# Kernel tuning notes

Hardware: AMD Instinct MI355X
Metric: run time of the kernel (lower is better)

The kernel has to match this reference:

```python
import jax, jax.numpy as jnp
import numpy as np

D = 256
BN_EPS = 1e-5
EPS = 0.0  # GINEEConv eps buffer, train_eps=False


def setup_inputs() -> dict:
    key = jax.random.key(0)
    ks = jax.random.split(key, 16)
    N, E, G = 60000, 200000, 1500
    node_features = jax.random.normal(ks[0], (N, 92), dtype=jnp.float32)
    edge_index = jax.random.randint(ks[1], (2, E), 0, N)
    atom_weights = jax.random.normal(ks[2], (E, 1), dtype=jnp.float32)
    batch = jnp.sort(jax.random.randint(ks[3], (N,), 0, G))
    s = 0.05
    return {
        "node_features": node_features,
        "edge_index": edge_index,
        "atom_weights": atom_weights,
        "batch": batch,
        "aW": jax.random.normal(ks[4], (92, D), dtype=jnp.float32) * s,
        "ab": jnp.zeros((D,), jnp.float32),
        "eW": jax.random.normal(ks[5], (1, D), dtype=jnp.float32) * s,
        "eb": jnp.zeros((D,), jnp.float32),
        "mlpW": jax.random.normal(ks[6], (3 * D, D), dtype=jnp.float32) * s,
        "mlpb": jnp.zeros((D,), jnp.float32),
        "nnW": jax.random.normal(ks[7], (D, D), dtype=jnp.float32) * s,
        "nnb": jnp.zeros((D,), jnp.float32),
        "bn_g": jax.random.normal(ks[8], (D,), dtype=jnp.float32) * 0.1 + 1.0,
        "bn_b": jax.random.normal(ks[9], (D,), dtype=jnp.float32) * 0.1,
        "bn_m": jax.random.normal(ks[10], (D,), dtype=jnp.float32) * 0.1,
        "bn_v": jax.random.uniform(ks[11], (D,), dtype=jnp.float32) + 0.5,
        "outW": jax.random.normal(ks[12], (D, 6), dtype=jnp.float32) * s,
        "outb": jnp.zeros((6,), jnp.float32),
    }


def _gine_layer(x, e_attr, row, col, mlpW, mlpb, nnW, nnb, bn_g, bn_b, bn_m, bn_v):
    # mlp(cat[x[row], x[col], e_attr]) without materializing the [E,3D] concat
    W1, W2, W3 = mlpW[:D], mlpW[D:2 * D], mlpW[2 * D:]
    new_e = x[row] @ W1 + x[col] @ W2 + e_attr @ W3 + mlpb  # [E, D]
    # message: relu(x_j + edge_attr), x_j = source nodes = edge_index[0]
    msg = jax.nn.relu(x[row] + new_e)  # [E, D]
    agg = jax.ops.segment_sum(msg, col, num_segments=x.shape[0])  # scatter-add to targets
    out = agg + (1.0 + EPS) * x  # residual
    h = out @ nnW + nnb
    h = (h - bn_m) * jax.lax.rsqrt(bn_v + BN_EPS) * bn_g + bn_b  # BN (eval stats)
    return jax.nn.relu(h), new_e


def reference(node_features, edge_index, atom_weights, batch,
              aW, ab, eW, eb, mlpW, mlpb, nnW, nnb,
              bn_g, bn_b, bn_m, bn_v, outW, outb):
    row, col = edge_index[0], edge_index[1]
    x = node_features @ aW + ab            # [N, 256]
    e_attr = atom_weights @ eW + eb        # [E, 256]
    for _ in range(4):  # 4 layers SHARING the same params (ModuleList of same module)
        x, e_attr = _gine_layer(x, e_attr, row, col, mlpW, mlpb, nnW, nnb,
                                bn_g, bn_b, bn_m, bn_v)
    pooled = jax.ops.segment_sum(x, batch, num_segments=1500)  # global_add_pool
    return pooled @ outW + outb  # [G, 6]
```

## Files before the change

### kernel.cpp

```cpp
#include <hip/hip_runtime.h>
#include <stdint.h>

#define DD 256
#define NNODE 60000
#define MPAD 60032
#define NEDGE 200000
#define NGRAPH 1500
#define NCHUNK 59

typedef __bf16 bf16x8 __attribute__((ext_vector_type(8)));
typedef float f32x4 __attribute__((ext_vector_type(4)));
typedef unsigned short us8 __attribute__((ext_vector_type(8)));

__device__ __forceinline__ unsigned short f2bf(float f) {
    union { float f; unsigned int u; } v; v.f = f;
    unsigned int r = v.u + 0x7FFFu + ((v.u >> 16) & 1u);
    return (unsigned short)(r >> 16);
}
__device__ __forceinline__ float bf2f(unsigned short h) {
    union { unsigned int u; float f; } v; v.u = ((unsigned int)h) << 16;
    return v.f;
}
__device__ __forceinline__ void gload_lds16(const void* g, void* l) {
    __builtin_amdgcn_global_load_lds((const __attribute__((address_space(1))) void*)g,
                                     (__attribute__((address_space(3))) void*)l, 16, 0, 0);
}

__global__ __launch_bounds__(256) void prep_weights(const float* __restrict__ mlpW,
                                                    const float* __restrict__ nnW,
                                                    const float* __restrict__ aW,
                                                    const float* __restrict__ ab,
                                                    unsigned short* __restrict__ wc1,
                                                    unsigned short* __restrict__ wc2,
                                                    unsigned short* __restrict__ nnt,
                                                    unsigned short* __restrict__ aWt) {
    int idx = blockIdx.x * 256 + threadIdx.x;
    if (idx < 256 * 512) {
        int n = idx >> 9, k = idx & 511;
        float v1 = (k < 256) ? mlpW[k * DD + n] : mlpW[(k + 256) * DD + n];
        wc1[idx] = f2bf(v1);
        wc2[idx] = f2bf(mlpW[(k + 256) * DD + n]);
    }
    if (idx < 256 * 256) {
        int n = idx >> 8, k = idx & 255;
        nnt[idx] = f2bf(nnW[k * DD + n]);
    }
    if (idx < 256 * 96) {
        int n = idx / 96, k = idx - n * 96;
        float v = (k < 92) ? aW[k * DD + n] : (k == 92 ? ab[n] : 0.0f);
        aWt[idx] = f2bf(v);
    }
}

__global__ __launch_bounds__(256) void prep_uv(const float* __restrict__ eW, const float* __restrict__ eb,
                                               const float* __restrict__ mlpW, const float* __restrict__ mlpb,
                                               const float* __restrict__ nnb,
                                               const float* __restrict__ bn_g, const float* __restrict__ bn_b,
                                               const float* __restrict__ bn_m, const float* __restrict__ bn_v,
                                               float* __restrict__ u_all, float* __restrict__ v_all,
                                               float* __restrict__ scale, float* __restrict__ shift) {
    __shared__ float uc[DD], vc[DD];
    int d = threadIdx.x;
    uc[d] = eW[d];
    vc[d] = eb[d];
    float sc = bn_g[d] * rsqrtf(bn_v[d] + 1e-5f);
    scale[d] = sc;
    shift[d] = (nnb[d] - bn_m[d]) * sc + bn_b[d];
    __syncthreads();
    const float* W3 = mlpW + 2 * DD * DD;
    for (int it = 0; it < 4; ++it) {
        float su = 0.f, sv = 0.f;
        for (int k = 0; k < DD; ++k) {
            float w = W3[k * DD + d];
            su += uc[k] * w;
            sv += vc[k] * w;
        }
        sv += mlpb[d];
        u_all[it * DD + d] = su;
        v_all[it * DD + d] = sv;
        __syncthreads();
        uc[d] = su; vc[d] = sv;
        __syncthreads();
    }
}

__global__ __launch_bounds__(256) void nfb_prep(const float* __restrict__ nf, unsigned short* __restrict__ nfb) {
    int idx = blockIdx.x * 256 + threadIdx.x;
    if (idx >= MPAD * 96) return;
    int r = idx / 96, c = idx - r * 96;
    float v;
    if (r < NNODE && c < 92) v = nf[(size_t)r * 92 + c];
    else v = (c == 92) ? 1.0f : 0.0f;
    nfb[idx] = f2bf(v);
}

__global__ __launch_bounds__(512) void xinit_gemm(const unsigned short* __restrict__ nfb,
                                                  const unsigned short* __restrict__ aWt,
                                                  unsigned short* __restrict__ x) {
    __shared__ unsigned short As[128][96];
    __shared__ unsigned short Bs[256][96];
    const int tid = threadIdx.x;
    const int lane = tid & 63, wid = tid >> 6;
    const int wr = wid >> 2, wc = wid & 3;
    const int m0 = blockIdx.x * 128;
    const int lr = lane & 15, lq = lane >> 4;

    for (int i = tid; i < 128 * 12; i += 512) {
        int row = i / 12, ch = (i - row * 12) * 8;
        gload_lds16(nfb + (size_t)(m0 + row) * 96 + ch, &As[row][ch]);
    }
    for (int i = tid; i < 256 * 12; i += 512) {
        int row = i / 12, ch = (i - row * 12) * 8;
        gload_lds16(aWt + (size_t)row * 96 + ch, &Bs[row][ch]);
    }
    __syncthreads();

    f32x4 acc[4][4];
    #pragma unroll
    for (int m = 0; m < 4; ++m)
        #pragma unroll
        for (int n = 0; n < 4; ++n) { f32x4 z = {0.f,0.f,0.f,0.f}; acc[m][n] = z; }

    #pragma unroll
    for (int h = 0; h < 3; ++h) {
        bf16x8 af[4], bf[4];
        #pragma unroll
        for (int m = 0; m < 4; ++m)
            af[m] = *reinterpret_cast<const bf16x8*>(&As[wr * 64 + m * 16 + lr][h * 32 + lq * 8]);
        #pragma unroll
        for (int n = 0; n < 4; ++n)
            bf[n] = *reinterpret_cast<const bf16x8*>(&Bs[wc * 64 + n * 16 + lr][h * 32 + lq * 8]);
        #pragma unroll
        for (int m = 0; m < 4; ++m)
            #pragma unroll
            for (int n = 0; n < 4; ++n)
                acc[m][n] = __builtin_amdgcn_mfma_f32_16x16x32_bf16(af[m], bf[n], acc[m][n], 0, 0, 0);
    }

    #pragma unroll
    for (int m = 0; m < 4; ++m) {
        const int rb = m0 + wr * 64 + m * 16 + lq * 4;
        #pragma unroll
        for (int n = 0; n < 4; ++n) {
            const int c = wc * 64 + n * 16 + lr;
            #pragma unroll
            for (int j = 0; j < 4; ++j)
                x[(size_t)(rb + j) * DD + c] = f2bf(acc[m][n][j]);
        }
    }
}

__global__ __launch_bounds__(256) void hist_kernel(const int* __restrict__ ei, int* __restrict__ counts) {
    int e = blockIdx.x * 256 + threadIdx.x;
    if (e < NEDGE) atomicAdd(&counts[ei[NEDGE + e]], 1);
}

__global__ __launch_bounds__(256) void scan1(const int* __restrict__ counts, int* __restrict__ blockSums) {
    int t = threadIdx.x;
    int base = blockIdx.x * 1024 + t * 4;
    int s = 0;
    #pragma unroll
    for (int i = 0; i < 4; ++i) { int idx = base + i; if (idx < NNODE) s += counts[idx]; }
    __shared__ int red[256];
    red[t] = s; __syncthreads();
    for (int d = 128; d; d >>= 1) { if (t < d) red[t] += red[t + d]; __syncthreads(); }
    if (t == 0) blockSums[blockIdx.x] = red[0];
}

__global__ __launch_bounds__(64) void scan2(int* __restrict__ blockSums) {
    int t = threadIdx.x;
    int v = (t < NCHUNK) ? blockSums[t] : 0;
    int orig = v;
    #pragma unroll
    for (int d = 1; d < 64; d <<= 1) {
        int o = __shfl_up(v, d);
        if (t >= d) v += o;
    }
    if (t < NCHUNK) blockSums[t] = v - orig;
}

__global__ __launch_bounds__(256) void scan3(const int* __restrict__ counts, const int* __restrict__ blockSums,
                                             int* __restrict__ offsets, int* __restrict__ cursor) {
    int t = threadIdx.x;
    int base = blockIdx.x * 1024 + t * 4;
    int c[4]; int s = 0;
    #pragma unroll
    for (int i = 0; i < 4; ++i) { int idx = base + i; c[i] = (idx < NNODE) ? counts[idx] : 0; s += c[i]; }
    __shared__ int lds[256];
    lds[t] = s; __syncthreads();
    for (int d = 1; d < 256; d <<= 1) {
        int v = (t >= d) ? lds[t - d] : 0;
        __syncthreads();
        lds[t] += v;
        __syncthreads();
    }
    int off = blockSums[blockIdx.x] + lds[t] - s;
    #pragma unroll
    for (int i = 0; i < 4; ++i) {
        int idx = base + i;
        if (idx < NNODE) { offsets[idx] = off; cursor[idx] = off; off += c[i]; }
    }
}

__global__ __launch_bounds__(256) void scatter_kernel(const int* __restrict__ ei, const float* __restrict__ aw,
                                                      int* __restrict__ cursor,
                                                      int* __restrict__ srow, float* __restrict__ sw) {
    int e = blockIdx.x * 256 + threadIdx.x;
    if (e < NEDGE) {
        int c = ei[NEDGE + e];
        int pos = atomicAdd(&cursor[c], 1);
        srow[pos] = ei[e];
        sw[pos] = aw[e];
    }
}

template <int EPI>
__global__ __launch_bounds__(512) void gemm_kernel(
    const unsigned short* __restrict__ A0,
    const unsigned short* __restrict__ A1,
    const unsigned short* __restrict__ Bt, int btStride, int Ktot,
    unsigned short* __restrict__ Cout,
    const float* __restrict__ scale, const float* __restrict__ shift) {
    __shared__ unsigned short As[128][64];
    __shared__ unsigned short Bs[256][64];
    const int tid = threadIdx.x;
    const int lane = tid & 63, wid = tid >> 6;
    const int wr = wid >> 2, wc = wid & 3;
    const int m0 = blockIdx.x * 128;
    const int lr = lane & 15, lq = lane >> 4;
    const int srow = tid >> 3;
    const int jphys = tid & 7;
    const int jlog = jphys ^ (srow & 7);
    const int scol_g = jlog * 8;
    const int scol_l = jphys * 8;
    const int xorj = (lr & 7);

    f32x4 acc[4][4];
    #pragma unroll
    for (int m = 0; m < 4; ++m)
        #pragma unroll
        for (int n = 0; n < 4; ++n) { f32x4 z = {0.f,0.f,0.f,0.f}; acc[m][n] = z; }

    const int nk = Ktot >> 6;
    for (int kt = 0; kt < nk; ++kt) {
        const int k0 = kt << 6;
        const unsigned short* Ap; int ka;
        if (k0 < 256) { Ap = A0; ka = k0; } else { Ap = A1; ka = k0 - 256; }
        #pragma unroll
        for (int p = 0; p < 2; ++p) {
            int row = p * 64 + srow;
            gload_lds16(Ap + (size_t)(m0 + row) * DD + ka + scol_g, &As[row][scol_l]);
        }
        #pragma unroll
        for (int p = 0; p < 4; ++p) {
            int row = p * 64 + srow;
            gload_lds16(Bt + (size_t)row * btStride + k0 + scol_g, &Bs[row][scol_l]);
        }
        __syncthreads();
        #pragma unroll
        for (int h = 0; h < 2; ++h) {
            const int jp = ((h * 4 + lq) ^ xorj) * 8;
            bf16x8 af[4], bfr[4];
            #pragma unroll
            for (int m = 0; m < 4; ++m)
                af[m] = *reinterpret_cast<const bf16x8*>(&As[wr * 64 + m * 16 + lr][jp]);
            #pragma unroll
            for (int n = 0; n < 4; ++n)
                bfr[n] = *reinterpret_cast<const bf16x8*>(&Bs[wc * 64 + n * 16 + lr][jp]);
            #pragma unroll
            for (int m = 0; m < 4; ++m)
                #pragma unroll
                for (int n = 0; n < 4; ++n)
                    acc[m][n] = __builtin_amdgcn_mfma_f32_16x16x32_bf16(af[m], bfr[n], acc[m][n], 0, 0, 0);
        }
        __syncthreads();
    }

    #pragma unroll
    for (int m = 0; m < 4; ++m) {
        const int rb = m0 + wr * 64 + m * 16 + lq * 4;
        #pragma unroll
        for (int n = 0; n < 4; ++n) {
            const int c = wc * 64 + n * 16 + lr;
            #pragma unroll
            for (int j = 0; j < 4; ++j) {
                const size_t idx = (size_t)(rb + j) * DD + c;
                if (EPI == 0) {
                    Cout[idx] = f2bf(acc[m][n][j]);
                } else {
                    float y = fmaxf(acc[m][n][j] * scale[c] + shift[c], 0.f);
                    Cout[idx] = f2bf(y);
                }
            }
        }
    }
}

__global__ __launch_bounds__(256) void edge_csr(const int* __restrict__ offsets, const int* __restrict__ counts,
                                                const int* __restrict__ srow, const float* __restrict__ sw,
                                                const unsigned short* __restrict__ X,
                                                const unsigned short* __restrict__ P,
                                                const unsigned short* __restrict__ Q,
                                                const float* __restrict__ u, const float* __restrict__ v,
                                                unsigned short* __restrict__ aggB) {
    const int lane = threadIdx.x & 63, wid = threadIdx.x >> 6;
    const int n = blockIdx.x * 4 + wid;
    if (n >= NNODE) return;
    const int start = offsets[n];
    const int deg = counts[n];
    const int sub = lane & 31, h = lane >> 5;

    const us8* X8 = (const us8*)X;
    const us8* P8 = (const us8*)P;

    float4 u0 = ((const float4*)u)[sub * 2], u1 = ((const float4*)u)[sub * 2 + 1];
    float4 v0 = ((const float4*)v)[sub * 2], v1 = ((const float4*)v)[sub * 2 + 1];
    float uu[8] = {u0.x, u0.y, u0.z, u0.w, u1.x, u1.y, u1.z, u1.w};
    float vv[8] = {v0.x, v0.y, v0.z, v0.w, v1.x, v1.y, v1.z, v1.w};

    us8 qv = ((const us8*)Q)[(size_t)n * 32 + sub];
    float base[8];
    #pragma unroll
    for (int c = 0; c < 8; ++c) base[c] = bf2f(qv[c]) + vv[c];

    float a[8];
    us8 xv = X8[(size_t)n * 32 + sub];
    #pragma unroll
    for (int c = 0; c < 8; ++c) a[c] = (h == 0) ? bf2f(xv[c]) : 0.f;

    for (int b0 = 0; b0 < deg; b0 += 64) {
        int m = deg - b0; if (m > 64) m = 64;
        int myr = 0; float myw = 0.f;
        if (lane < m) { myr = srow[start + b0 + lane]; myw = sw[start + b0 + lane]; }
        int iters = (m + 1) >> 1;
        for (int j = 0; j < iters; ++j) {
            int el = 2 * j + h;
            int r = __shfl(myr, el);
            float w = __shfl(myw, el);
            if (el < m) {
                us8 x2 = X8[(size_t)r * 32 + sub];
                us8 p2 = P8[(size_t)r * 32 + sub];
                #pragma unroll
                for (int c = 0; c < 8; ++c)
                    a[c] += fmaxf(bf2f(x2[c]) + bf2f(p2[c]) + base[c] + w * uu[c], 0.f);
            }
        }
    }
    #pragma unroll
    for (int c = 0; c < 8; ++c) a[c] += __shfl_xor(a[c], 32);
    if (h == 0) {
        us8 o;
        #pragma unroll
        for (int c = 0; c < 8; ++c) o[c] = f2bf(a[c]);
        ((us8*)aggB)[(size_t)n * 32 + sub] = o;
    }
}

__global__ __launch_bounds__(256) void pool_kernel(const unsigned short* __restrict__ x,
                                                   const int* __restrict__ batch,
                                                   float* __restrict__ pooled) {
    const int lane = threadIdx.x & 63, wid = threadIdx.x >> 6;
    const int base = (blockIdx.x * 4 + wid) * 8;
    float4 acc = make_float4(0.f, 0.f, 0.f, 0.f);
    int gcur = -1;
    for (int i = 0; i < 8; ++i) {
        int n = base + i;
        if (n >= NNODE) break;
        int g = batch[n];
        if (g != gcur) {
            if (gcur >= 0) {
                float* pp = pooled + (size_t)gcur * DD + lane * 4;
                unsafeAtomicAdd(pp + 0, acc.x);
                unsafeAtomicAdd(pp + 1, acc.y);
                unsafeAtomicAdd(pp + 2, acc.z);
                unsafeAtomicAdd(pp + 3, acc.w);
            }
            gcur = g;
            acc = make_float4(0.f, 0.f, 0.f, 0.f);
        }
        ushort4 xv = ((const ushort4*)x)[(size_t)n * 64 + lane];
        acc.x += bf2f(xv.x); acc.y += bf2f(xv.y);
        acc.z += bf2f(xv.z); acc.w += bf2f(xv.w);
    }
    if (gcur >= 0) {
        float* pp = pooled + (size_t)gcur * DD + lane * 4;
        unsafeAtomicAdd(pp + 0, acc.x);
        unsafeAtomicAdd(pp + 1, acc.y);
        unsafeAtomicAdd(pp + 2, acc.z);
        unsafeAtomicAdd(pp + 3, acc.w);
    }
}

__global__ __launch_bounds__(64) void out_kernel(const float* __restrict__ pooled,
                                                 const float* __restrict__ outW,
                                                 const float* __restrict__ outb,
                                                 float* __restrict__ out) {
    const int g = blockIdx.x, lane = threadIdx.x;
    float4 p = ((const float4*)pooled)[g * 64 + lane];
    float s[6];
    #pragma unroll
    for (int j = 0; j < 6; ++j) {
        float a = p.x * outW[(lane * 4 + 0) * 6 + j] + p.y * outW[(lane * 4 + 1) * 6 + j] +
                  p.z * outW[(lane * 4 + 2) * 6 + j] + p.w * outW[(lane * 4 + 3) * 6 + j];
        #pragma unroll
        for (int off = 32; off; off >>= 1) a += __shfl_down(a, off);
        s[j] = a;
    }
    if (lane == 0) {
        #pragma unroll
        for (int j = 0; j < 6; ++j) out[g * 6 + j] = s[j] + outb[j];
    }
}

extern "C" void kernel_launch(void* const* d_in, const int* in_sizes, int n_in,
                              void* d_out, int out_size, void* d_ws, size_t ws_size,
                              hipStream_t stream) {
    const float* nf    = (const float*)d_in[0];
    const int*   ei    = (const int*)d_in[1];
    const float* aw    = (const float*)d_in[2];
    const int*   batch = (const int*)d_in[3];
    const float* aW    = (const float*)d_in[4];
    const float* ab    = (const float*)d_in[5];
    const float* eW    = (const float*)d_in[6];
    const float* eb    = (const float*)d_in[7];
    const float* mlpW  = (const float*)d_in[8];
    const float* mlpb  = (const float*)d_in[9];
    const float* nnW   = (const float*)d_in[10];
    const float* nnb   = (const float*)d_in[11];
    const float* bn_g  = (const float*)d_in[12];
    const float* bn_b  = (const float*)d_in[13];
    const float* bn_m  = (const float*)d_in[14];
    const float* bn_v  = (const float*)d_in[15];
    const float* outW  = (const float*)d_in[16];
    const float* outb  = (const float*)d_in[17];
    float* out = (float*)d_out;

    char* ws = (char*)d_ws;
    size_t off = 0;
    auto alloc = [&](size_t bytes) -> void* {
        void* p = ws + off;
        off += (bytes + 255) & ~(size_t)255;
        return p;
    };
    unsigned short* x    = (unsigned short*)alloc((size_t)MPAD * DD * 2);
    unsigned short* P    = (unsigned short*)alloc((size_t)MPAD * DD * 2);
    unsigned short* Q    = (unsigned short*)alloc((size_t)MPAD * DD * 2);
    unsigned short* aggB = (unsigned short*)alloc((size_t)MPAD * DD * 2);
    unsigned short* nfb  = (unsigned short*)alloc((size_t)MPAD * 96 * 2);
    unsigned short* wc1  = (unsigned short*)alloc(256 * 512 * 2);
    unsigned short* wc2  = (unsigned short*)alloc(256 * 512 * 2);
    unsigned short* nnt  = (unsigned short*)alloc(256 * 256 * 2);
    unsigned short* aWt  = (unsigned short*)alloc(256 * 96 * 2);
    float* u_all = (float*)alloc(4 * DD * 4);
    float* v_all = (float*)alloc(4 * DD * 4);
    float* scale = (float*)alloc(DD * 4);
    float* shift = (float*)alloc(DD * 4);
    float* pooled = (float*)alloc((size_t)NGRAPH * DD * 4);
    int* counts  = (int*)alloc((size_t)NNODE * 4);
    int* offsets = (int*)alloc((size_t)NNODE * 4);
    int* cursor  = (int*)alloc((size_t)NNODE * 4);
    int* blockSums = (int*)alloc(NCHUNK * 4);
    int* srowB   = (int*)alloc((size_t)NEDGE * 4);
    float* swB   = (float*)alloc((size_t)NEDGE * 4);
    (void)ws_size; (void)in_sizes; (void)n_in; (void)out_size;

    prep_weights<<<512, 256, 0, stream>>>(mlpW, nnW, aW, ab, wc1, wc2, nnt, aWt);
    prep_uv<<<1, 256, 0, stream>>>(eW, eb, mlpW, mlpb, nnb, bn_g, bn_b, bn_m, bn_v,
                                   u_all, v_all, scale, shift);
    nfb_prep<<<(MPAD * 96 + 255) / 256, 256, 0, stream>>>(nf, nfb);
    xinit_gemm<<<MPAD / 128, 512, 0, stream>>>(nfb, aWt, x);

    hipMemsetAsync(counts, 0, (size_t)NNODE * 4, stream);
    hist_kernel<<<(NEDGE + 255) / 256, 256, 0, stream>>>(ei, counts);
    scan1<<<NCHUNK, 256, 0, stream>>>(counts, blockSums);
    scan2<<<1, 64, 0, stream>>>(blockSums);
    scan3<<<NCHUNK, 256, 0, stream>>>(counts, blockSums, offsets, cursor);
    scatter_kernel<<<(NEDGE + 255) / 256, 256, 0, stream>>>(ei, aw, cursor, srowB, swB);

    for (int k = 0; k < 4; ++k) {
        int Ktot = k ? 512 : 256;
        gemm_kernel<0><<<MPAD / 128, 512, 0, stream>>>(x, k ? P : nullptr, wc1, 512, Ktot,
                                                       P, nullptr, nullptr);
        gemm_kernel<0><<<MPAD / 128, 512, 0, stream>>>(x, k ? Q : nullptr, wc2, 512, Ktot,
                                                       Q, nullptr, nullptr);
        edge_csr<<<(NNODE + 3) / 4, 256, 0, stream>>>(offsets, counts, srowB, swB, x, P, Q,
                                                      u_all + k * DD, v_all + k * DD, aggB);
        gemm_kernel<1><<<MPAD / 128, 512, 0, stream>>>(aggB, nullptr, nnt, 256, 256,
                                                       x, scale, shift);
    }

    hipMemsetAsync(pooled, 0, (size_t)NGRAPH * DD * 4, stream);
    pool_kernel<<<(NNODE + 31) / 32, 256, 0, stream>>>(x, batch, pooled);
    out_kernel<<<NGRAPH, 64, 0, stream>>>(pooled, outW, outb, out);
}
```

Measured before the change: 519.6 us.

## Fuse P/Q GEMMs into one launch and precompute P+X for edge gather

The two per-layer P and Q GEMMs become one launch whose block index interleaves P and Q tiles for the same rows, so the shared X tile is more likely to be reused from L2. The P epilogue also writes PX = P + X, and the per-layer bias is folded into Q. The edge aggregation kernel then gathers one neighbor row (PX) per edge instead of two (X and P), roughly halving its random gather traffic. The cost is an extra full-size PX write per layer, and the input buffer for the initial node features is aliased onto the PX buffer.

```diff
diff --git a/kernel.cpp b/kernel.cpp
--- a/kernel.cpp
+++ b/kernel.cpp
@@ -214,13 +214,111 @@
     }
 }
 
-template <int EPI>
-__global__ __launch_bounds__(512) void gemm_kernel(
-    const unsigned short* __restrict__ A0,
-    const unsigned short* __restrict__ A1,
-    const unsigned short* __restrict__ Bt, int btStride, int Ktot,
-    unsigned short* __restrict__ Cout,
-    const float* __restrict__ scale, const float* __restrict__ shift) {
+__global__ __launch_bounds__(512) void gemm_pq(const unsigned short* __restrict__ X,
+                                               const unsigned short* __restrict__ Pst,
+                                               const unsigned short* __restrict__ Qst,
+                                               const unsigned short* __restrict__ B1,
+                                               const unsigned short* __restrict__ B2,
+                                               unsigned short* __restrict__ Pout,
+                                               unsigned short* __restrict__ PXout,
+                                               unsigned short* __restrict__ Qout,
+                                               const float* __restrict__ cq,
+                                               int Ktot) {
+    __shared__ unsigned short As[128][64];
+    __shared__ unsigned short Bs[256][64];
+    const int b = blockIdx.x;
+    const int pairb = b >> 4, jj = b & 15;
+    const int sel = jj >> 3, sub = jj & 7;
+    const int mb = pairb * 8 + sub;
+    if (mb >= MPAD / 128) return;
+    const int m0 = mb * 128;
+
+    const unsigned short* A1 = sel ? Qst : Pst;
+    const unsigned short* Bt = sel ? B2 : B1;
+
+    const int tid = threadIdx.x;
+    const int lane = tid & 63, wid = tid >> 6;
+    const int wr = wid >> 2, wc = wid & 3;
+    const int lr = lane & 15, lq = lane >> 4;
+    const int srow = tid >> 3;
+    const int jphys = tid & 7;
+    const int jlog = jphys ^ (srow & 7);
+    const int scol_g = jlog * 8;
+    const int scol_l = jphys * 8;
+    const int xorj = (lr & 7);
+
+    f32x4 acc[4][4];
+    #pragma unroll
+    for (int m = 0; m < 4; ++m)
+        #pragma unroll
+        for (int n = 0; n < 4; ++n) { f32x4 z = {0.f,0.f,0.f,0.f}; acc[m][n] = z; }
+
+    const int nk = Ktot >> 6;
+    for (int kt = 0; kt < nk; ++kt) {
+        const int k0 = kt << 6;
+        const unsigned short* Ap; int ka;
+        if (k0 < 256) { Ap = X; ka = k0; } else { Ap = A1; ka = k0 - 256; }
+        #pragma unroll
+        for (int p = 0; p < 2; ++p) {
+            int row = p * 64 + srow;
+            gload_lds16(Ap + (size_t)(m0 + row) * DD + ka + scol_g, &As[row][scol_l]);
+        }
+        #pragma unroll
+        for (int p = 0; p < 4; ++p) {
+            int row = p * 64 + srow;
+            gload_lds16(Bt + (size_t)row * 512 + k0 + scol_g, &Bs[row][scol_l]);
+        }
+        __syncthreads();
+        #pragma unroll
+        for (int h = 0; h < 2; ++h) {
+            const int jp = ((h * 4 + lq) ^ xorj) * 8;
+            bf16x8 af[4], bfr[4];
+            #pragma unroll
+            for (int m = 0; m < 4; ++m)
+                af[m] = *reinterpret_cast<const bf16x8*>(&As[wr * 64 + m * 16 + lr][jp]);
+            #pragma unroll
+            for (int n = 0; n < 4; ++n)
+                bfr[n] = *reinterpret_cast<const bf16x8*>(&Bs[wc * 64 + n * 16 + lr][jp]);
+            #pragma unroll
+            for (int m = 0; m < 4; ++m)
+                #pragma unroll
+                for (int n = 0; n < 4; ++n)
+                    acc[m][n] = __builtin_amdgcn_mfma_f32_16x16x32_bf16(af[m], bfr[n], acc[m][n], 0, 0, 0);
+        }
+        __syncthreads();
+    }
+
+    #pragma unroll
+    for (int m = 0; m < 4; ++m) {
+        const int rb = m0 + wr * 64 + m * 16 + lq * 4;
+        #pragma unroll
+        for (int n = 0; n < 4; ++n) {
+            const int c = wc * 64 + n * 16 + lr;
+            if (sel == 0) {
+                #pragma unroll
+                for (int j = 0; j < 4; ++j) {
+                    const size_t idx = (size_t)(rb + j) * DD + c;
+                    float cv = acc[m][n][j];
+                    Pout[idx] = f2bf(cv);
+                    PXout[idx] = f2bf(cv + bf2f(X[idx]));
+                }
+            } else {
+                const float cqc = cq[c];
+                #pragma unroll
+                for (int j = 0; j < 4; ++j) {
+                    const size_t idx = (size_t)(rb + j) * DD + c;
+                    Qout[idx] = f2bf(acc[m][n][j] + cqc);
+                }
+            }
+        }
+    }
+}
+
+__global__ __launch_bounds__(512) void gemm_bn(const unsigned short* __restrict__ A,
+                                               const unsigned short* __restrict__ Bt,
+                                               unsigned short* __restrict__ Cout,
+                                               const float* __restrict__ scale,
+                                               const float* __restrict__ shift) {
     __shared__ unsigned short As[128][64];
     __shared__ unsigned short Bs[256][64];
     const int tid = threadIdx.x;
@@ -241,20 +339,17 @@
         #pragma unroll
         for (int n = 0; n < 4; ++n) { f32x4 z = {0.f,0.f,0.f,0.f}; acc[m][n] = z; }
 
-    const int nk = Ktot >> 6;
-    for (int kt = 0; kt < nk; ++kt) {
+    for (int kt = 0; kt < 4; ++kt) {
         const int k0 = kt << 6;
-        const unsigned short* Ap; int ka;
-        if (k0 < 256) { Ap = A0; ka = k0; } else { Ap = A1; ka = k0 - 256; }
         #pragma unroll
         for (int p = 0; p < 2; ++p) {
             int row = p * 64 + srow;
-            gload_lds16(Ap + (size_t)(m0 + row) * DD + ka + scol_g, &As[row][scol_l]);
+            gload_lds16(A + (size_t)(m0 + row) * DD + k0 + scol_g, &As[row][scol_l]);
         }
         #pragma unroll
         for (int p = 0; p < 4; ++p) {
             int row = p * 64 + srow;
-            gload_lds16(Bt + (size_t)row * btStride + k0 + scol_g, &Bs[row][scol_l]);
+            gload_lds16(Bt + (size_t)row * DD + k0 + scol_g, &Bs[row][scol_l]);
         }
         __syncthreads();
         #pragma unroll
@@ -285,12 +380,8 @@
             #pragma unroll
             for (int j = 0; j < 4; ++j) {
                 const size_t idx = (size_t)(rb + j) * DD + c;
-                if (EPI == 0) {
-                    Cout[idx] = f2bf(acc[m][n][j]);
-                } else {
-                    float y = fmaxf(acc[m][n][j] * scale[c] + shift[c], 0.f);
-                    Cout[idx] = f2bf(y);
-                }
+                float y = fmaxf(acc[m][n][j] * scale[c] + shift[c], 0.f);
+                Cout[idx] = f2bf(y);
             }
         }
     }
@@ -299,9 +390,9 @@
 __global__ __launch_bounds__(256) void edge_csr(const int* __restrict__ offsets, const int* __restrict__ counts,
                                                 const int* __restrict__ srow, const float* __restrict__ sw,
                                                 const unsigned short* __restrict__ X,
-                                                const unsigned short* __restrict__ P,
-                                                const unsigned short* __restrict__ Q,
-                                                const float* __restrict__ u, const float* __restrict__ v,
+                                                const unsigned short* __restrict__ PX,
+                                                const unsigned short* __restrict__ Qv,
+                                                const float* __restrict__ u,
                                                 unsigned short* __restrict__ aggB) {
     const int lane = threadIdx.x & 63, wid = threadIdx.x >> 6;
     const int n = blockIdx.x * 4 + wid;
@@ -310,21 +401,18 @@
     const int deg = counts[n];
     const int sub = lane & 31, h = lane >> 5;
 
-    const us8* X8 = (const us8*)X;
-    const us8* P8 = (const us8*)P;
+    const us8* PX8 = (const us8*)PX;
 
     float4 u0 = ((const float4*)u)[sub * 2], u1 = ((const float4*)u)[sub * 2 + 1];
-    float4 v0 = ((const float4*)v)[sub * 2], v1 = ((const float4*)v)[sub * 2 + 1];
     float uu[8] = {u0.x, u0.y, u0.z, u0.w, u1.x, u1.y, u1.z, u1.w};
-    float vv[8] = {v0.x, v0.y, v0.z, v0.w, v1.x, v1.y, v1.z, v1.w};
-
-    us8 qv = ((const us8*)Q)[(size_t)n * 32 + sub];
-    float base[8];
-    #pragma unroll
-    for (int c = 0; c < 8; ++c) base[c] = bf2f(qv[c]) + vv[c];
+
+    us8 qv = ((const us8*)Qv)[(size_t)n * 32 + sub];
+    float qb[8];
+    #pragma unroll
+    for (int c = 0; c < 8; ++c) qb[c] = bf2f(qv[c]);
 
     float a[8];
-    us8 xv = X8[(size_t)n * 32 + sub];
+    us8 xv = ((const us8*)X)[(size_t)n * 32 + sub];
     #pragma unroll
     for (int c = 0; c < 8; ++c) a[c] = (h == 0) ? bf2f(xv[c]) : 0.f;
 
@@ -338,11 +426,10 @@
             int r = __shfl(myr, el);
             float w = __shfl(myw, el);
             if (el < m) {
-                us8 x2 = X8[(size_t)r * 32 + sub];
-                us8 p2 = P8[(size_t)r * 32 + sub];
+                us8 p2 = PX8[(size_t)r * 32 + sub];
                 #pragma unroll
                 for (int c = 0; c < 8; ++c)
-                    a[c] += fmaxf(bf2f(x2[c]) + bf2f(p2[c]) + base[c] + w * uu[c], 0.f);
+                    a[c] += fmaxf(bf2f(p2[c]) + qb[c] + w * uu[c], 0.f);
             }
         }
     }
@@ -444,9 +531,10 @@
     };
     unsigned short* x    = (unsigned short*)alloc((size_t)MPAD * DD * 2);
     unsigned short* P    = (unsigned short*)alloc((size_t)MPAD * DD * 2);
-    unsigned short* Q    = (unsigned short*)alloc((size_t)MPAD * DD * 2);
+    unsigned short* Qv   = (unsigned short*)alloc((size_t)MPAD * DD * 2);
     unsigned short* aggB = (unsigned short*)alloc((size_t)MPAD * DD * 2);
-    unsigned short* nfb  = (unsigned short*)alloc((size_t)MPAD * 96 * 2);
+    unsigned short* PX   = (unsigned short*)alloc((size_t)MPAD * DD * 2);
+    unsigned short* nfb  = PX;
     unsigned short* wc1  = (unsigned short*)alloc(256 * 512 * 2);
     unsigned short* wc2  = (unsigned short*)alloc(256 * 512 * 2);
     unsigned short* nnt  = (unsigned short*)alloc(256 * 256 * 2);
@@ -477,16 +565,13 @@
     scan3<<<NCHUNK, 256, 0, stream>>>(counts, blockSums, offsets, cursor);
     scatter_kernel<<<(NEDGE + 255) / 256, 256, 0, stream>>>(ei, aw, cursor, srowB, swB);
 
+    const int npairs = (MPAD / 128 + 7) / 8;
     for (int k = 0; k < 4; ++k) {
-        int Ktot = k ? 512 : 256;
-        gemm_kernel<0><<<MPAD / 128, 512, 0, stream>>>(x, k ? P : nullptr, wc1, 512, Ktot,
-                                                       P, nullptr, nullptr);
-        gemm_kernel<0><<<MPAD / 128, 512, 0, stream>>>(x, k ? Q : nullptr, wc2, 512, Ktot,
-                                                       Q, nullptr, nullptr);
-        edge_csr<<<(NNODE + 3) / 4, 256, 0, stream>>>(offsets, counts, srowB, swB, x, P, Q,
-                                                      u_all + k * DD, v_all + k * DD, aggB);
-        gemm_kernel<1><<<MPAD / 128, 512, 0, stream>>>(aggB, nullptr, nnt, 256, 256,
-                                                       x, scale, shift);
+        gemm_pq<<<npairs * 16, 512, 0, stream>>>(x, P, Qv, wc1, wc2, P, PX, Qv,
+                                                 k == 0 ? v_all : mlpb, k ? 512 : 256);
+        edge_csr<<<(NNODE + 3) / 4, 256, 0, stream>>>(offsets, counts, srowB, swB, x, PX, Qv,
+                                                      u_all + k * DD, aggB);
+        gemm_bn<<<MPAD / 128, 512, 0, stream>>>(aggB, nnt, x, scale, shift);
     }
 
     hipMemsetAsync(pooled, 0, (size_t)NGRAPH * DD * 4, stream);
```

New measurement: 518.2 us. No clear change (-0.3%).
